# Performance work log

Measured on AMD Instinct MI355X. Metric: run time of the kernel, lower is better.

Reference implementation:

```python
import jax, jax.numpy as jnp
import numpy as np

DIM = 1024
H = 16          # query heads
HKV = 4         # kv heads
HD = DIM // H   # head_dim = 64
B = 8           # equal-length docs
S = 1024        # tokens per doc
N = B * S       # total tokens
ROPE_BASE = 10000.0


def _rms_norm(x, scale):
    eps = jnp.asarray(jnp.finfo(x.dtype).eps, x.dtype)
    inv = jax.lax.rsqrt(jnp.mean(x * x, axis=-1, keepdims=True) + eps)
    return x * inv * scale


def _rope(x, cos, sin):
    # x: [N, h, HD]; cos/sin: [N, 1, HD//2]
    half = x.shape[-1] // 2
    x1, x2 = x[..., :half], x[..., half:]
    return jnp.concatenate((x1 * cos + x2 * sin, -x1 * sin + x2 * cos), axis=-1)


def setup_inputs() -> dict:
    key = jax.random.key(0)
    ks = jax.random.split(key, 8)
    x = jax.random.normal(ks[0], (N, DIM), dtype=jnp.float32)
    Wq = jax.random.normal(ks[1], (DIM, DIM), dtype=jnp.float32) * (DIM ** -0.5)
    Wk = jax.random.normal(ks[2], (HKV * HD, DIM), dtype=jnp.float32) * (DIM ** -0.5)
    Wv = jax.random.normal(ks[3], (HKV * HD, DIM), dtype=jnp.float32) * (DIM ** -0.5)
    Wproj = jax.random.normal(ks[4], (DIM, DIM), dtype=jnp.float32) * (DIM ** -0.5)
    q_gain = jnp.full((H,), 1.0, dtype=jnp.float32)
    q_scale = jnp.asarray(1.0, dtype=jnp.float32)  # q RMSNorm scale
    k_scale = jnp.asarray(1.0, dtype=jnp.float32)  # k RMSNorm scale
    # rotary tables per Rotary.prepare_positions (positions reset per doc)
    cu_seqlens = jnp.arange(B + 1, dtype=jnp.int32) * S
    positions = jnp.tile(jnp.arange(S, dtype=jnp.float32), B)  # [N]
    inv_freq = 1.0 / (ROPE_BASE ** (jnp.arange(0, HD, 2, dtype=jnp.float32) / HD))
    freqs = positions[:, None] * inv_freq[None, :]  # [N, HD//2]
    rotary_cos = jnp.cos(freqs)[:, None, :]
    rotary_sin = jnp.sin(freqs)[:, None, :]
    return {
        "x": x, "Wq": Wq, "Wk": Wk, "Wv": Wv, "Wproj": Wproj,
        "q_gain": q_gain, "q_scale": q_scale, "k_scale": k_scale,
        "rotary_cos": rotary_cos, "rotary_sin": rotary_sin,
        "cu_seqlens": cu_seqlens, "max_doc_len": S,
    }


def reference(x, Wq, Wk, Wv, Wproj, q_gain, q_scale, k_scale,
              rotary_cos, rotary_sin, cu_seqlens, max_doc_len):
    n_tokens, dim = x.shape
    q = (x @ Wq.T).reshape(n_tokens, H, HD)
    k = (x @ Wk.T).reshape(n_tokens, HKV, HD)
    v = (x @ Wv.T).reshape(n_tokens, HKV, HD)
    q = _rms_norm(q, q_scale)
    k = _rms_norm(k, k_scale)
    q = _rope(q, rotary_cos, rotary_sin)
    k = _rope(k, rotary_cos, rotary_sin)
    q = q * q_gain[None, :, None]
    # equal-length docs -> [B, S, h, HD]; GQA: repeat kv heads
    rep = H // HKV
    qb = q.reshape(B, S, H, HD)
    kb = jnp.repeat(k.reshape(B, S, HKV, HD), rep, axis=2)
    vb = jnp.repeat(v.reshape(B, S, HKV, HD), rep, axis=2)
    scale = HD ** -0.5
    scores = jnp.einsum('bqhd,bkhd->bhqk', qb, kb) * scale  # [B,H,S,S]
    causal = jnp.tril(jnp.ones((S, S), dtype=bool))
    scores = jnp.where(causal[None, None], scores, jnp.asarray(-jnp.inf, scores.dtype))
    attn = jax.nn.softmax(scores, axis=-1)
    y = jnp.einsum('bhqk,bkhd->bqhd', attn, vb).reshape(n_tokens, dim)
    return y @ Wproj.T
```

## Files before the change

### kernel.cpp

```cpp
#include <hip/hip_runtime.h>
#include <hip/hip_bf16.h>


typedef __bf16 bf16x8 __attribute__((ext_vector_type(8)));
typedef float f32x4 __attribute__((ext_vector_type(4)));

__device__ __forceinline__ void async16(const void* g, void* l) {
  __builtin_amdgcn_global_load_lds((const __attribute__((address_space(1))) void*)g,
                                   (__attribute__((address_space(3))) void*)l, 16, 0, 0);
}

__device__ __forceinline__ unsigned short f2bfu(float x) {
  __hip_bfloat16 h = __float2bfloat16(x);
  return __builtin_bit_cast(unsigned short, h);
}

__global__ __launch_bounds__(256) void castall(
    const float4* __restrict__ x, const float4* __restrict__ Wq,
    const float4* __restrict__ Wk, const float4* __restrict__ Wv,
    const float4* __restrict__ Wp,
    ushort4* __restrict__ xb, ushort4* __restrict__ w1b, ushort4* __restrict__ wpb) {
  int i = blockIdx.x * 256 + threadIdx.x;
  const float4* src;
  ushort4* dst;
  if (i < 2097152)      { src = x + i;             dst = xb + i; }
  else if (i < 2359296) { src = Wq + (i - 2097152); dst = w1b + (i - 2097152); }
  else if (i < 2424832) { src = Wk + (i - 2359296); dst = w1b + (i - 2097152); }
  else if (i < 2490368) { src = Wv + (i - 2424832); dst = w1b + (i - 2097152); }
  else                  { src = Wp + (i - 2490368); dst = wpb + (i - 2490368); }
  float4 v = *src;
  ushort4 o;
  o.x = f2bfu(v.x); o.y = f2bfu(v.y); o.z = f2bfu(v.z); o.w = f2bfu(v.w);
  *dst = o;
}

__global__ __launch_bounds__(256, 3) void gemm_qkv(
    const __hip_bfloat16* __restrict__ A,
    const __hip_bfloat16* __restrict__ Bm,
    const float* __restrict__ cosb, const float* __restrict__ sinb,
    const float* __restrict__ qgain, const float* __restrict__ qscale,
    const float* __restrict__ kscale,
    __hip_bfloat16* __restrict__ Qo,
    __hip_bfloat16* __restrict__ Ko,
    __hip_bfloat16* __restrict__ Vo)
{
  __shared__ __align__(16) unsigned short As[128 * 32];
  __shared__ __align__(16) unsigned short Bs[128 * 32];
  const int tid = threadIdx.x;
  const int wave = tid >> 6, lane = tid & 63;
  const int quad = lane >> 4, l15 = lane & 15;
  const int bn = blockIdx.x, bm = blockIdx.y;
  const int wm = (wave >> 1) * 64, wn = (wave & 1) * 64;
  const int srow = lane >> 2, scol = (lane & 3) * 8;
  const int K = 1024;

  f32x4 acc[4][4] = {};

  const __hip_bfloat16* Ab = A + (size_t)bm * 128 * K;
  const __hip_bfloat16* Bb = Bm + (size_t)bn * 128 * K;

  for (int kt = 0; kt < K; kt += 32) {
    __syncthreads();
#pragma unroll
    for (int c = 0; c < 2; c++) {
      const int ch = wave * 2 + c;
      async16(Ab + (size_t)(ch * 16 + srow) * K + kt + scol, &As[ch * 512]);
      async16(Bb + (size_t)(ch * 16 + srow) * K + kt + scol, &Bs[ch * 512]);
    }
    __syncthreads();
    bf16x8 af[4], bfr[4];
#pragma unroll
    for (int mt = 0; mt < 4; mt++)
      af[mt] = *(const bf16x8*)&As[(wm + mt * 16 + l15) * 32 + quad * 8];
#pragma unroll
    for (int nt = 0; nt < 4; nt++)
      bfr[nt] = *(const bf16x8*)&Bs[(wn + nt * 16 + l15) * 32 + quad * 8];
#pragma unroll
    for (int mt = 0; mt < 4; mt++)
#pragma unroll
      for (int nt = 0; nt < 4; nt++)
        acc[mt][nt] = __builtin_amdgcn_mfma_f32_16x16x32_bf16(af[mt], bfr[nt], acc[mt][nt], 0, 0, 0);
  }

  const int hg = bn * 2 + (wn >> 6);
  const int tokbase = bm * 128 + wm;

  if (hg >= 20) {
    const int hv = hg - 20;
#pragma unroll
    for (int mt = 0; mt < 4; mt++)
#pragma unroll
      for (int r = 0; r < 4; r++) {
        const int tok = tokbase + mt * 16 + quad * 4 + r;
#pragma unroll
        for (int nt = 0; nt < 4; nt++)
          Vo[(size_t)tok * 256 + hv * 64 + nt * 16 + l15] = __float2bfloat16(acc[mt][nt][r]);
      }
  } else {
    const bool isq = hg < 16;
    const float scale = isq ? qscale[0] : kscale[0];
    const float gain = isq ? qgain[hg] : 1.0f;
    const float sg = scale * gain;
#pragma unroll
    for (int mt = 0; mt < 4; mt++) {
      float inv[4];
#pragma unroll
      for (int r = 0; r < 4; r++) {
        float ss = acc[mt][0][r] * acc[mt][0][r] + acc[mt][1][r] * acc[mt][1][r] +
                   acc[mt][2][r] * acc[mt][2][r] + acc[mt][3][r] * acc[mt][3][r];
#pragma unroll
        for (int off = 1; off < 16; off <<= 1) ss += __shfl_xor(ss, off);
        inv[r] = rsqrtf(ss * (1.0f / 64.0f) + 1.1920929e-07f) * sg;
      }
#pragma unroll
      for (int r = 0; r < 4; r++) {
        const int tok = tokbase + mt * 16 + quad * 4 + r;
        const float c0 = cosb[tok * 32 + l15], c1 = cosb[tok * 32 + 16 + l15];
        const float s0 = sinb[tok * 32 + l15], s1 = sinb[tok * 32 + 16 + l15];
        const float v0 = acc[mt][0][r] * inv[r];
        const float v1 = acc[mt][1][r] * inv[r];
        const float v2 = acc[mt][2][r] * inv[r];
        const float v3 = acc[mt][3][r] * inv[r];
        const float o0 = v0 * c0 + v2 * s0;
        const float o1 = v1 * c1 + v3 * s1;
        const float o2 = -v0 * s0 + v2 * c0;
        const float o3 = -v1 * s1 + v3 * c1;
        __hip_bfloat16* base = isq ? (Qo + (size_t)tok * 1024 + hg * 64)
                                   : (Ko + (size_t)tok * 256 + (hg - 16) * 64);
        base[l15]      = __float2bfloat16(o0);
        base[16 + l15] = __float2bfloat16(o1);
        base[32 + l15] = __float2bfloat16(o2);
        base[48 + l15] = __float2bfloat16(o3);
      }
    }
  }
}

__global__ __launch_bounds__(256, 4) void gemm_p(
    const __hip_bfloat16* __restrict__ A,
    const __hip_bfloat16* __restrict__ Bm,
    float* __restrict__ C)
{
  __shared__ __align__(16) unsigned short As[128 * 32];
  __shared__ __align__(16) unsigned short Bs[64 * 32];
  const int tid = threadIdx.x;
  const int wave = tid >> 6, lane = tid & 63;
  const int quad = lane >> 4, l15 = lane & 15;
  const int bn = blockIdx.x, bm = blockIdx.y;
  const int wm = wave * 32;
  const int srow = lane >> 2, scol = (lane & 3) * 8;
  const int K = 1024;

  f32x4 acc[2][4] = {};

  const __hip_bfloat16* Ab = A + (size_t)bm * 128 * K;
  const __hip_bfloat16* Bb = Bm + (size_t)bn * 64 * K;

  for (int kt = 0; kt < K; kt += 32) {
    __syncthreads();
#pragma unroll
    for (int c = 0; c < 2; c++) {
      const int ch = wave * 2 + c;
      async16(Ab + (size_t)(ch * 16 + srow) * K + kt + scol, &As[ch * 512]);
    }
    async16(Bb + (size_t)(wave * 16 + srow) * K + kt + scol, &Bs[wave * 512]);
    __syncthreads();
    bf16x8 af[2], bfr[4];
#pragma unroll
    for (int mt = 0; mt < 2; mt++)
      af[mt] = *(const bf16x8*)&As[(wm + mt * 16 + l15) * 32 + quad * 8];
#pragma unroll
    for (int nt = 0; nt < 4; nt++)
      bfr[nt] = *(const bf16x8*)&Bs[(nt * 16 + l15) * 32 + quad * 8];
#pragma unroll
    for (int mt = 0; mt < 2; mt++)
#pragma unroll
      for (int nt = 0; nt < 4; nt++)
        acc[mt][nt] = __builtin_amdgcn_mfma_f32_16x16x32_bf16(af[mt], bfr[nt], acc[mt][nt], 0, 0, 0);
  }

#pragma unroll
  for (int mt = 0; mt < 2; mt++)
#pragma unroll
    for (int nt = 0; nt < 4; nt++)
#pragma unroll
      for (int r = 0; r < 4; r++) {
        const int row = bm * 128 + wm + mt * 16 + quad * 4 + r;
        const int col = bn * 64 + nt * 16 + l15;
        C[(size_t)row * 1024 + col] = acc[mt][nt][r];
      }
}

__global__ __launch_bounds__(256) void vtrans(const unsigned short* __restrict__ vkb,
                                              unsigned short* __restrict__ Vt) {
  __shared__ unsigned short t[64][65];
  const int st = blockIdx.x, kvh = blockIdx.y, b = blockIdx.z;
  const int tid = threadIdx.x;
  const int s0 = st * 64;
#pragma unroll
  for (int i = 0; i < 16; i++) {
    const int idx = tid + i * 256;
    const int sl = idx >> 6, d = idx & 63;
    t[sl][d] = vkb[(size_t)(b * 1024 + s0 + sl) * 256 + kvh * 64 + d];
  }
  __syncthreads();
#pragma unroll
  for (int i = 0; i < 16; i++) {
    const int idx = tid + i * 256;
    const int d = idx >> 6, sl = idx & 63;
    Vt[((size_t)(b * 4 + kvh) * 64 + d) * 1024 + s0 + sl] = t[sl][d];
  }
}

__global__ __launch_bounds__(512, 4) void attn(
    const __hip_bfloat16* __restrict__ Q,
    const __hip_bfloat16* __restrict__ Kk,
    const __hip_bfloat16* __restrict__ Vt,
    __hip_bfloat16* __restrict__ Y)
{
  __shared__ __align__(16) unsigned short Kb[2][4096];
  __shared__ __align__(16) unsigned short Vb[2][4096];
  __shared__ __align__(16) unsigned short Pm[8][32 * 72];
  __shared__ float Lsh[8][32];

  const int xx = blockIdx.x;
  const int qt = (xx & 1) ? (xx >> 1) : (15 - (xx >> 1));
  const int kvh = blockIdx.y, b = blockIdx.z;
  const int tid = threadIdx.x;
  const int wave = tid >> 6, lane = tid & 63;
  const int quad = lane >> 4, l15 = lane & 15;
  const int h = kvh * 4 + (wave >> 1);
  const int m0 = (wave & 1) * 32;
  const int tok0 = b * 1024 + qt * 64;

  const int srow = lane >> 2;
  const int scol = (lane & 3) * 8;

  bf16x8 qf[2][2];
#pragma unroll
  for (int mt = 0; mt < 2; mt++)
#pragma unroll
    for (int kc = 0; kc < 2; kc++)
      qf[mt][kc] = *(const bf16x8*)(Q + (size_t)(tok0 + m0 + mt * 16 + l15) * 1024 +
                                    h * 64 + kc * 32 + quad * 8);

  auto issue = [&](int kt, unsigned short* Ks, unsigned short* Vs) {
#pragma unroll
    for (int c = 0; c < 2; c++) {
      const int ch = wave * 2 + c;
      const int v = ch >> 3;
      const int ch8 = ch & 7;
      const int kc = ch8 >> 2, grp = ch8 & 3;
      if (v == 0)
        async16(Kk + (size_t)(b * 1024 + kt * 64 + grp * 16 + srow) * 256 + kvh * 64 + kc * 32 + scol,
                Ks + kc * 2048 + grp * 512 + lane * 8);
      else
        async16(Vt + ((size_t)((b * 4 + kvh) * 64 + grp * 16 + srow)) * 1024 + kt * 64 + kc * 32 + scol,
                Vs + kc * 2048 + grp * 512 + lane * 8);
    }
  };

  issue(0, Kb[0], Vb[0]);

  f32x4 of[2][4] = {};
  float lsum[2] = {0.0f, 0.0f};
  const float scl2 = 0.125f * 1.44269504089f;
  unsigned short* Pw = Pm[wave];

  for (int kt = 0; kt <= qt; kt++) {
    __syncthreads();
    if (kt < qt) issue(kt + 1, Kb[(kt + 1) & 1], Vb[(kt + 1) & 1]);
    const unsigned short* Ks = Kb[kt & 1];
    const unsigned short* Vs = Vb[kt & 1];

    f32x4 sf[4][2] = {};
#pragma unroll
    for (int kc = 0; kc < 2; kc++) {
#pragma unroll
      for (int kk = 0; kk < 4; kk++) {
        const bf16x8 kf = *(const bf16x8*)&Ks[kc * 2048 + (kk * 16 + l15) * 32 + quad * 8];
#pragma unroll
        for (int mt = 0; mt < 2; mt++)
          sf[kk][mt] = __builtin_amdgcn_mfma_f32_16x16x32_bf16(kf, qf[mt][kc], sf[kk][mt], 0, 0, 0);
      }
    }

    const bool diag = (kt == qt);
#pragma unroll
    for (int mt = 0; mt < 2; mt++) {
#pragma unroll
      for (int kk = 0; kk < 4; kk++) {
        ushort4 pk;
        unsigned short* pp = (unsigned short*)&pk;
#pragma unroll
        for (int r = 0; r < 4; r++) {
          float p;
          if (diag && (kk * 16 + quad * 4 + r) > (m0 + mt * 16 + l15)) {
            p = 0.0f;
          } else {
            p = __builtin_amdgcn_exp2f(sf[kk][mt][r] * scl2);
          }
          lsum[mt] += p;
          pp[r] = f2bfu(p);
        }
        *(ushort4*)&Pw[(mt * 16 + l15) * 72 + kk * 16 + quad * 4] = pk;
      }
    }

    asm volatile("s_waitcnt lgkmcnt(0)" ::: "memory");

#pragma unroll
    for (int kc = 0; kc < 2; kc++) {
#pragma unroll
      for (int mt = 0; mt < 2; mt++) {
        const bf16x8 ap = *(const bf16x8*)&Pw[(mt * 16 + l15) * 72 + kc * 32 + quad * 8];
#pragma unroll
        for (int dt = 0; dt < 4; dt++) {
          const bf16x8 bv = *(const bf16x8*)&Vs[kc * 2048 + (dt * 16 + l15) * 32 + quad * 8];
          of[mt][dt] = __builtin_amdgcn_mfma_f32_16x16x32_bf16(ap, bv, of[mt][dt], 0, 0, 0);
        }
      }
    }
  }

#pragma unroll
  for (int mt = 0; mt < 2; mt++) {
    float l = lsum[mt];
    l += __shfl_xor(l, 16);
    l += __shfl_xor(l, 32);
    Lsh[wave][mt * 16 + l15] = l;
  }
  asm volatile("s_waitcnt lgkmcnt(0)" ::: "memory");

#pragma unroll
  for (int mt = 0; mt < 2; mt++)
#pragma unroll
    for (int r = 0; r < 4; r++) {
      const float rcp = 1.0f / Lsh[wave][mt * 16 + quad * 4 + r];
      const int row = tok0 + m0 + mt * 16 + quad * 4 + r;
#pragma unroll
      for (int dt = 0; dt < 4; dt++)
        Y[(size_t)row * 1024 + h * 64 + dt * 16 + l15] = __float2bfloat16(of[mt][dt][r] * rcp);
    }
}

extern "C" void kernel_launch(void* const* d_in, const int* in_sizes, int n_in,
                              void* d_out, int out_size, void* d_ws, size_t ws_size,
                              hipStream_t stream) {
  const float* x      = (const float*)d_in[0];
  const float* Wq     = (const float*)d_in[1];
  const float* Wk     = (const float*)d_in[2];
  const float* Wv     = (const float*)d_in[3];
  const float* Wp     = (const float*)d_in[4];
  const float* qgain  = (const float*)d_in[5];
  const float* qscale = (const float*)d_in[6];
  const float* kscale = (const float*)d_in[7];
  const float* cosb   = (const float*)d_in[8];
  const float* sinb   = (const float*)d_in[9];
  float* out = (float*)d_out;
  char* ws = (char*)d_ws;

  __hip_bfloat16* xb  = (__hip_bfloat16*)(ws);
  __hip_bfloat16* w1b = (__hip_bfloat16*)(ws + 16777216);
  __hip_bfloat16* wpb = (__hip_bfloat16*)(ws + 19922944);
  __hip_bfloat16* qb  = (__hip_bfloat16*)(ws + 22020096);
  __hip_bfloat16* kb  = (__hip_bfloat16*)(ws + 38797312);
  __hip_bfloat16* vkb = (__hip_bfloat16*)(ws + 42991616);
  __hip_bfloat16* vtb = (__hip_bfloat16*)(ws + 47185920);
  __hip_bfloat16* yb  = (__hip_bfloat16*)(ws + 51380224);

  castall<<<10752, 256, 0, stream>>>((const float4*)x, (const float4*)Wq, (const float4*)Wk,
                                     (const float4*)Wv, (const float4*)Wp,
                                     (ushort4*)xb, (ushort4*)w1b, (ushort4*)wpb);

  gemm_qkv<<<dim3(12, 64), 256, 0, stream>>>(xb, w1b, cosb, sinb, qgain, qscale, kscale,
                                             qb, kb, vkb);

  vtrans<<<dim3(16, 4, 8), 256, 0, stream>>>((const unsigned short*)vkb, (unsigned short*)vtb);

  attn<<<dim3(16, 4, 8), 512, 0, stream>>>(qb, kb, vtb, yb);

  gemm_p<<<dim3(16, 64), 256, 0, stream>>>(yb, wpb, out);
}
```

Measured before the change: 221.2 us.

## Pair causal query tiles per attention block, fold softmax scale into Q, widen proj GEMM tile

The attention kernel now gives each 256-thread block two query tiles (qt and 15-qt) for two heads, so every block does the same amount of causal work. The softmax scale and log2e are folded into q_gain in the QKV epilogue, and row sums are computed by an MFMA against a ones vector instead of scalar adds and shuffles. MFMA sections are wrapped in s_setprio. The output projection GEMM moves to 128x128 tiles with 4x4 MFMA per wave, which raises reuse but lowers occupancy.

```diff
diff --git a/kernel.cpp b/kernel.cpp
--- a/kernel.cpp
+++ b/kernel.cpp
@@ -99,7 +99,7 @@
   } else {
     const bool isq = hg < 16;
     const float scale = isq ? qscale[0] : kscale[0];
-    const float gain = isq ? qgain[hg] : 1.0f;
+    const float gain = isq ? qgain[hg] * 0.18033688011112042f : 1.0f;
     const float sg = scale * gain;
 #pragma unroll
     for (int mt = 0; mt < 4; mt++) {
@@ -136,25 +136,25 @@
   }
 }
 
-__global__ __launch_bounds__(256, 4) void gemm_p(
+__global__ __launch_bounds__(256, 3) void gemm_p(
     const __hip_bfloat16* __restrict__ A,
     const __hip_bfloat16* __restrict__ Bm,
     float* __restrict__ C)
 {
   __shared__ __align__(16) unsigned short As[128 * 32];
-  __shared__ __align__(16) unsigned short Bs[64 * 32];
+  __shared__ __align__(16) unsigned short Bs[128 * 32];
   const int tid = threadIdx.x;
   const int wave = tid >> 6, lane = tid & 63;
   const int quad = lane >> 4, l15 = lane & 15;
   const int bn = blockIdx.x, bm = blockIdx.y;
-  const int wm = wave * 32;
+  const int wm = (wave >> 1) * 64, wn = (wave & 1) * 64;
   const int srow = lane >> 2, scol = (lane & 3) * 8;
   const int K = 1024;
 
-  f32x4 acc[2][4] = {};
+  f32x4 acc[4][4] = {};
 
   const __hip_bfloat16* Ab = A + (size_t)bm * 128 * K;
-  const __hip_bfloat16* Bb = Bm + (size_t)bn * 64 * K;
+  const __hip_bfloat16* Bb = Bm + (size_t)bn * 128 * K;
 
   for (int kt = 0; kt < K; kt += 32) {
     __syncthreads();
@@ -162,33 +162,32 @@
     for (int c = 0; c < 2; c++) {
       const int ch = wave * 2 + c;
       async16(Ab + (size_t)(ch * 16 + srow) * K + kt + scol, &As[ch * 512]);
-    }
-    async16(Bb + (size_t)(wave * 16 + srow) * K + kt + scol, &Bs[wave * 512]);
+      async16(Bb + (size_t)(ch * 16 + srow) * K + kt + scol, &Bs[ch * 512]);
+    }
     __syncthreads();
-    bf16x8 af[2], bfr[4];
-#pragma unroll
-    for (int mt = 0; mt < 2; mt++)
+    bf16x8 af[4], bfr[4];
+#pragma unroll
+    for (int mt = 0; mt < 4; mt++)
       af[mt] = *(const bf16x8*)&As[(wm + mt * 16 + l15) * 32 + quad * 8];
 #pragma unroll
     for (int nt = 0; nt < 4; nt++)
-      bfr[nt] = *(const bf16x8*)&Bs[(nt * 16 + l15) * 32 + quad * 8];
-#pragma unroll
-    for (int mt = 0; mt < 2; mt++)
+      bfr[nt] = *(const bf16x8*)&Bs[(wn + nt * 16 + l15) * 32 + quad * 8];
+#pragma unroll
+    for (int mt = 0; mt < 4; mt++)
 #pragma unroll
       for (int nt = 0; nt < 4; nt++)
         acc[mt][nt] = __builtin_amdgcn_mfma_f32_16x16x32_bf16(af[mt], bfr[nt], acc[mt][nt], 0, 0, 0);
   }
 
 #pragma unroll
-  for (int mt = 0; mt < 2; mt++)
-#pragma unroll
-    for (int nt = 0; nt < 4; nt++)
-#pragma unroll
-      for (int r = 0; r < 4; r++) {
-        const int row = bm * 128 + wm + mt * 16 + quad * 4 + r;
-        const int col = bn * 64 + nt * 16 + l15;
-        C[(size_t)row * 1024 + col] = acc[mt][nt][r];
-      }
+  for (int mt = 0; mt < 4; mt++)
+#pragma unroll
+    for (int r = 0; r < 4; r++) {
+      const int row = bm * 128 + wm + mt * 16 + quad * 4 + r;
+#pragma unroll
+      for (int nt = 0; nt < 4; nt++)
+        C[(size_t)row * 1024 + bn * 128 + wn + nt * 16 + l15] = acc[mt][nt][r];
+    }
 }
 
 __global__ __launch_bounds__(256) void vtrans(const unsigned short* __restrict__ vkb,
@@ -212,7 +211,7 @@
   }
 }
 
-__global__ __launch_bounds__(512, 4) void attn(
+__global__ __launch_bounds__(256, 2) void attn(
     const __hip_bfloat16* __restrict__ Q,
     const __hip_bfloat16* __restrict__ Kk,
     const __hip_bfloat16* __restrict__ Vt,
@@ -220,34 +219,24 @@
 {
   __shared__ __align__(16) unsigned short Kb[2][4096];
   __shared__ __align__(16) unsigned short Vb[2][4096];
-  __shared__ __align__(16) unsigned short Pm[8][32 * 72];
-  __shared__ float Lsh[8][32];
-
-  const int xx = blockIdx.x;
-  const int qt = (xx & 1) ? (xx >> 1) : (15 - (xx >> 1));
-  const int kvh = blockIdx.y, b = blockIdx.z;
+  __shared__ __align__(16) unsigned short Pm[4][32 * 72];
+
+  const int p = blockIdx.x;
+  const int qt_a = 15 - p, qt_b = p;
+  const int kvh2 = blockIdx.y;
+  const int kvh = kvh2 >> 1, hh = kvh2 & 1;
+  const int b = blockIdx.z;
   const int tid = threadIdx.x;
   const int wave = tid >> 6, lane = tid & 63;
   const int quad = lane >> 4, l15 = lane & 15;
-  const int h = kvh * 4 + (wave >> 1);
+  const int h = kvh * 4 + hh * 2 + (wave >> 1);
   const int m0 = (wave & 1) * 32;
-  const int tok0 = b * 1024 + qt * 64;
-
-  const int srow = lane >> 2;
-  const int scol = (lane & 3) * 8;
-
-  bf16x8 qf[2][2];
-#pragma unroll
-  for (int mt = 0; mt < 2; mt++)
-#pragma unroll
-    for (int kc = 0; kc < 2; kc++)
-      qf[mt][kc] = *(const bf16x8*)(Q + (size_t)(tok0 + m0 + mt * 16 + l15) * 1024 +
-                                    h * 64 + kc * 32 + quad * 8);
+  const int srow = lane >> 2, scol = (lane & 3) * 8;
 
   auto issue = [&](int kt, unsigned short* Ks, unsigned short* Vs) {
 #pragma unroll
-    for (int c = 0; c < 2; c++) {
-      const int ch = wave * 2 + c;
+    for (int c = 0; c < 4; c++) {
+      const int ch = wave * 4 + c;
       const int v = ch >> 3;
       const int ch8 = ch & 7;
       const int kc = ch8 >> 2, grp = ch8 & 3;
@@ -260,20 +249,55 @@
     }
   };
 
+  bf16x8 qf[2][2];
+  {
+    const int tok0 = b * 1024 + qt_a * 64;
+#pragma unroll
+    for (int mt = 0; mt < 2; mt++)
+#pragma unroll
+      for (int kc = 0; kc < 2; kc++)
+        qf[mt][kc] = *(const bf16x8*)(Q + (size_t)(tok0 + m0 + mt * 16 + l15) * 1024 +
+                                      h * 64 + kc * 32 + quad * 8);
+  }
+
   issue(0, Kb[0], Vb[0]);
 
   f32x4 of[2][4] = {};
-  float lsum[2] = {0.0f, 0.0f};
-  const float scl2 = 0.125f * 1.44269504089f;
+  f32x4 lf[2] = {};
   unsigned short* Pw = Pm[wave];
 
-  for (int kt = 0; kt <= qt; kt++) {
+  bf16x8 onesf;
+#pragma unroll
+  for (int j = 0; j < 8; j++) onesf[j] = (__bf16)1.0f;
+
+  const int steps_a = qt_a + 1;
+  const int total = steps_a + qt_b + 1;
+
+  for (int g = 0; g < total; ++g) {
+    const bool pa = g < steps_a;
+    const int qtc = pa ? qt_a : qt_b;
+    const int kt = pa ? g : g - steps_a;
+
     __syncthreads();
-    if (kt < qt) issue(kt + 1, Kb[(kt + 1) & 1], Vb[(kt + 1) & 1]);
-    const unsigned short* Ks = Kb[kt & 1];
-    const unsigned short* Vs = Vb[kt & 1];
+    if (g + 1 < total) {
+      const int gn = g + 1;
+      const int ktn = (gn < steps_a) ? gn : gn - steps_a;
+      issue(ktn, Kb[gn & 1], Vb[gn & 1]);
+    }
+    if (g == steps_a) {
+      const int tok0 = b * 1024 + qt_b * 64;
+#pragma unroll
+      for (int mt = 0; mt < 2; mt++)
+#pragma unroll
+        for (int kc = 0; kc < 2; kc++)
+          qf[mt][kc] = *(const bf16x8*)(Q + (size_t)(tok0 + m0 + mt * 16 + l15) * 1024 +
+                                        h * 64 + kc * 32 + quad * 8);
+    }
+    const unsigned short* Ks = Kb[g & 1];
+    const unsigned short* Vs = Vb[g & 1];
 
     f32x4 sf[4][2] = {};
+    __builtin_amdgcn_s_setprio(1);
 #pragma unroll
     for (int kc = 0; kc < 2; kc++) {
 #pragma unroll
@@ -284,8 +308,9 @@
           sf[kk][mt] = __builtin_amdgcn_mfma_f32_16x16x32_bf16(kf, qf[mt][kc], sf[kk][mt], 0, 0, 0);
       }
     }
-
-    const bool diag = (kt == qt);
+    __builtin_amdgcn_s_setprio(0);
+
+    const bool diag = (kt == qtc);
 #pragma unroll
     for (int mt = 0; mt < 2; mt++) {
 #pragma unroll
@@ -294,14 +319,12 @@
         unsigned short* pp = (unsigned short*)&pk;
 #pragma unroll
         for (int r = 0; r < 4; r++) {
-          float p;
-          if (diag && (kk * 16 + quad * 4 + r) > (m0 + mt * 16 + l15)) {
-            p = 0.0f;
-          } else {
-            p = __builtin_amdgcn_exp2f(sf[kk][mt][r] * scl2);
-          }
-          lsum[mt] += p;
-          pp[r] = f2bfu(p);
+          float pv;
+          if (diag && (kk * 16 + quad * 4 + r) > (m0 + mt * 16 + l15))
+            pv = 0.0f;
+          else
+            pv = __builtin_amdgcn_exp2f(sf[kk][mt][r]);
+          pp[r] = f2bfu(pv);
         }
         *(ushort4*)&Pw[(mt * 16 + l15) * 72 + kk * 16 + quad * 4] = pk;
       }
@@ -309,11 +332,13 @@
 
     asm volatile("s_waitcnt lgkmcnt(0)" ::: "memory");
 
+    __builtin_amdgcn_s_setprio(1);
 #pragma unroll
     for (int kc = 0; kc < 2; kc++) {
 #pragma unroll
       for (int mt = 0; mt < 2; mt++) {
         const bf16x8 ap = *(const bf16x8*)&Pw[(mt * 16 + l15) * 72 + kc * 32 + quad * 8];
+        lf[mt] = __builtin_amdgcn_mfma_f32_16x16x32_bf16(ap, onesf, lf[mt], 0, 0, 0);
 #pragma unroll
         for (int dt = 0; dt < 4; dt++) {
           const bf16x8 bv = *(const bf16x8*)&Vs[kc * 2048 + (dt * 16 + l15) * 32 + quad * 8];
@@ -321,27 +346,30 @@
         }
       }
     }
-  }
-
-#pragma unroll
-  for (int mt = 0; mt < 2; mt++) {
-    float l = lsum[mt];
-    l += __shfl_xor(l, 16);
-    l += __shfl_xor(l, 32);
-    Lsh[wave][mt * 16 + l15] = l;
-  }
-  asm volatile("s_waitcnt lgkmcnt(0)" ::: "memory");
-
-#pragma unroll
-  for (int mt = 0; mt < 2; mt++)
-#pragma unroll
-    for (int r = 0; r < 4; r++) {
-      const float rcp = 1.0f / Lsh[wave][mt * 16 + quad * 4 + r];
-      const int row = tok0 + m0 + mt * 16 + quad * 4 + r;
-#pragma unroll
-      for (int dt = 0; dt < 4; dt++)
-        Y[(size_t)row * 1024 + h * 64 + dt * 16 + l15] = __float2bfloat16(of[mt][dt][r] * rcp);
-    }
+    __builtin_amdgcn_s_setprio(0);
+
+    if (diag) {
+      const int tok0 = b * 1024 + qtc * 64;
+#pragma unroll
+      for (int mt = 0; mt < 2; mt++)
+#pragma unroll
+        for (int r = 0; r < 4; r++) {
+          const float rcp = 1.0f / lf[mt][r];
+          const int row = tok0 + m0 + mt * 16 + quad * 4 + r;
+#pragma unroll
+          for (int dt = 0; dt < 4; dt++)
+            Y[(size_t)row * 1024 + h * 64 + dt * 16 + l15] = __float2bfloat16(of[mt][dt][r] * rcp);
+        }
+      if (pa) {
+#pragma unroll
+        for (int mt = 0; mt < 2; mt++) {
+          lf[mt] = f32x4{0.f, 0.f, 0.f, 0.f};
+#pragma unroll
+          for (int dt = 0; dt < 4; dt++) of[mt][dt] = f32x4{0.f, 0.f, 0.f, 0.f};
+        }
+      }
+    }
+  }
 }
 
 extern "C" void kernel_launch(void* const* d_in, const int* in_sizes, int n_in,
@@ -378,7 +406,7 @@
 
   vtrans<<<dim3(16, 4, 8), 256, 0, stream>>>((const unsigned short*)vkb, (unsigned short*)vtb);
 
-  attn<<<dim3(16, 4, 8), 512, 0, stream>>>(qb, kb, vtb, yb);
-
-  gemm_p<<<dim3(16, 64), 256, 0, stream>>>(yb, wpb, out);
-}
+  attn<<<dim3(8, 8, 8), 256, 0, stream>>>(qb, kb, vtb, yb);
+
+  gemm_p<<<dim3(8, 64), 256, 0, stream>>>(yb, wpb, out);
+}
```

After: 211.0 us. -4.6%, faster.
